# Optimization experiments

Measured on AMD Instinct MI355X. Metric: run time of the kernel, lower is better.

The kernel has to match this reference:

```python
import jax, jax.numpy as jnp
import numpy as np

B, G, IN, H, OUT = 4096, 8, 512, 1024, 64


def setup_inputs() -> dict:
    key = jax.random.key(0)
    k0, k1, k2, k3 = jax.random.split(key, 4)
    x = jax.random.normal(k0, (B, IN), dtype=jnp.float32)
    gid = jax.random.randint(k1, (B,), 0, G, dtype=jnp.int32)
    # Per-group 2-layer MLP params (Kaiming-ish scaling)
    W1 = jax.random.normal(k2, (G, IN, H), dtype=jnp.float32) / np.sqrt(IN)
    b1 = jnp.zeros((G, H), dtype=jnp.float32)
    W2 = jax.random.normal(k3, (G, H, OUT), dtype=jnp.float32) / np.sqrt(H)
    b2 = jnp.zeros((G, OUT), dtype=jnp.float32)
    return {"x": x, "gid": gid, "W1": W1, "b1": b1, "W2": W2, "b2": b2}


def reference(x, gid, W1, b1, W2, b2):
    # Routed 2-layer MLP: each sample i uses expert head gid[i].
    # Compute all G group GEMMs (grouped-GEMM style), then select the
    # routed row per sample with a one-hot contraction (no [B,IN,H]
    # per-sample weight materialization).
    onehot = jax.nn.one_hot(gid, W1.shape[0], dtype=x.dtype)  # [B, G]
    h_all = jnp.einsum('bi,gih->bgh', x, W1) + b1[None]       # [B, G, H]
    h = jax.nn.relu(jnp.einsum('bgh,bg->bh', h_all, onehot))  # [B, H]
    y_all = jnp.einsum('bh,gho->bgo', h, W2) + b2[None]       # [B, G, OUT]
    y = jnp.einsum('bgo,bg->bo', y_all, onehot)               # [B, OUT]
    return y
```

## Files before the change

kernel.cpp:

```cpp
#include <hip/hip_runtime.h>
#include <hip/hip_bf16.h>

#define B_ 4096
#define G_ 8
#define IN_ 512
#define H_ 1024
#define OUT_ 64
#define MAXT 72

typedef float f32x4 __attribute__((ext_vector_type(4)));
typedef __bf16 bf16x8 __attribute__((ext_vector_type(8)));
typedef unsigned short u16x8 __attribute__((ext_vector_type(8)));

__device__ inline unsigned short f2bf(float f) {
  unsigned int u = __builtin_bit_cast(unsigned int, f);
  u += 0x7fffu + ((u >> 16) & 1u);
  return (unsigned short)(u >> 16);
}

__device__ inline u16x8 pack8(float4 a, float4 b) {
  return u16x8{f2bf(a.x), f2bf(a.y), f2bf(a.z), f2bf(a.w),
               f2bf(b.x), f2bf(b.y), f2bf(b.z), f2bf(b.w)};
}

__device__ inline bool tile_lookup(const int* __restrict__ meta, int mt,
                                   int& g, int& row0, int& start, int& cnt) {
  int ts = 0;
  bool found = false;
#pragma unroll
  for (int gg = 0; gg < G_; gg++) {
    int s = meta[gg], e = meta[gg + 1];
    int T = (e - s + 63) >> 6;
    if (!found && mt >= ts && mt < ts + T) {
      g = gg;
      row0 = (mt - ts) << 6;
      start = s;
      cnt = e - s;
      found = true;
    }
    ts += T;
  }
  return found;
}

__global__ __launch_bounds__(256) void prep_kernel(
    const float* __restrict__ W1, const float* __restrict__ W2,
    const float* __restrict__ x, unsigned short* __restrict__ W1t,
    unsigned short* __restrict__ W2t, unsigned short* __restrict__ xb) {
  int b = blockIdx.x;
  int t = threadIdx.x;
  if (b < 4096) {
    __shared__ float tile[32][33];
    int h32 = b & 31, k32 = (b >> 5) & 15, g = b >> 9;
    int kl = t >> 3, nl = (t & 7) * 4;
    const float* src =
        W1 + ((size_t)g * IN_ + k32 * 32 + kl) * H_ + h32 * 32 + nl;
    float4 v = *(const float4*)src;
    tile[kl][nl + 0] = v.x;
    tile[kl][nl + 1] = v.y;
    tile[kl][nl + 2] = v.z;
    tile[kl][nl + 3] = v.w;
    __syncthreads();
    int nl2 = t >> 3, kl2 = (t & 7) * 4;
    ushort4 o;
    o.x = f2bf(tile[kl2 + 0][nl2]);
    o.y = f2bf(tile[kl2 + 1][nl2]);
    o.z = f2bf(tile[kl2 + 2][nl2]);
    o.w = f2bf(tile[kl2 + 3][nl2]);
    *(ushort4*)(W1t + ((size_t)g * H_ + h32 * 32 + nl2) * IN_ + k32 * 32 +
                kl2) = o;
  } else if (b < 4608) {
    __shared__ float tile2[32][33];
    int bb = b - 4096;
    int g = bb >> 6, k32 = (bb >> 1) & 31, n32 = bb & 1;
    int kl = t >> 3, nl = (t & 7) * 4;
    const float* src =
        W2 + ((size_t)g * H_ + k32 * 32 + kl) * OUT_ + n32 * 32 + nl;
    float4 v = *(const float4*)src;
    tile2[kl][nl + 0] = v.x;
    tile2[kl][nl + 1] = v.y;
    tile2[kl][nl + 2] = v.z;
    tile2[kl][nl + 3] = v.w;
    __syncthreads();
    int nl2 = t >> 3, kl2 = (t & 7) * 4;
    ushort4 o;
    o.x = f2bf(tile2[kl2 + 0][nl2]);
    o.y = f2bf(tile2[kl2 + 1][nl2]);
    o.z = f2bf(tile2[kl2 + 2][nl2]);
    o.w = f2bf(tile2[kl2 + 3][nl2]);
    *(ushort4*)(W2t + ((size_t)g * OUT_ + n32 * 32 + nl2) * H_ + k32 * 32 +
                kl2) = o;
  } else {
    int bb = b - 4608;
    size_t base = (size_t)bb * 2048 + t * 8;
    float4 v0 = *(const float4*)(x + base);
    float4 v1 = *(const float4*)(x + base + 4);
    *(u16x8*)(xb + base) = pack8(v0, v1);
  }
}

__global__ __launch_bounds__(256) void bucket_kernel(
    const int* __restrict__ gid, int* __restrict__ meta,
    int* __restrict__ perm) {
  __shared__ unsigned short lc[256][G_];
  __shared__ int offs_s[G_ + 1];
  int t = threadIdx.x;
#pragma unroll
  for (int g = 0; g < G_; g++) lc[t][g] = 0;
  int myg[16];
  const int base = t * 16;
#pragma unroll
  for (int j = 0; j < 16; j++) {
    myg[j] = gid[base + j];
    lc[t][myg[j]]++;
  }
  __syncthreads();
  if (t < G_) {
    int run = 0;
    for (int tt = 0; tt < 256; tt++) {
      int v = lc[tt][t];
      lc[tt][t] = (unsigned short)run;
      run += v;
    }
    offs_s[t + 1] = run;
  }
  __syncthreads();
  if (t == 0) {
    int o = 0;
    for (int g = 0; g < G_; g++) {
      int c = offs_s[g + 1];
      offs_s[g] = o;
      meta[g] = o;
      o += c;
    }
    offs_s[G_] = o;
    meta[G_] = o;
  }
  __syncthreads();
  int cur[G_];
#pragma unroll
  for (int g = 0; g < G_; g++) cur[g] = offs_s[g] + (int)lc[t][g];
#pragma unroll
  for (int j = 0; j < 16; j++) {
    int g = myg[j];
    perm[cur[g]++] = base + j;
  }
}

__global__ __launch_bounds__(256) void gemm1_kernel(
    const unsigned short* __restrict__ xb, const unsigned short* __restrict__ W1t,
    const float* __restrict__ b1, const int* __restrict__ meta,
    const int* __restrict__ perm, unsigned short* __restrict__ hb) {
  int b = blockIdx.x;
  int mt = b >> 4, nt = b & 15;
  int g, row0, start, cnt;
  if (!tile_lookup(meta, mt, g, row0, start, cnt)) return;
  int n0 = nt * 64;

  __shared__ __attribute__((aligned(16))) unsigned short As[64 * 64];
  __shared__ __attribute__((aligned(16))) unsigned short Bs[64 * 64];
  __shared__ int rows[64];

  int tid = threadIdx.x;
  int lane = tid & 63;
  int wv = tid >> 6;

  if (tid < 64) rows[tid] = perm[start + min(row0 + tid, cnt - 1)];
  __syncthreads();

  int r = tid >> 2, c4 = tid & 3;
  const unsigned short* xsrc = xb + (size_t)rows[r] * IN_ + c4 * 16;
  unsigned short* adst0 = &As[r * 64 + (((2 * c4) ^ (r & 7)) << 3)];
  unsigned short* adst1 = &As[r * 64 + (((2 * c4 + 1) ^ (r & 7)) << 3)];

  int brow0 = wv * 16 + (lane >> 3);
  int brow1 = brow0 + 8;
  int bsl = lane & 7;
  const unsigned short* bsrc0 = W1t + ((size_t)g * H_ + n0 + brow0) * IN_ +
                                ((bsl ^ (brow0 & 7)) << 3);
  const unsigned short* bsrc1 = W1t + ((size_t)g * H_ + n0 + brow1) * IN_ +
                                ((bsl ^ (brow1 & 7)) << 3);
  unsigned short* bdst0 = &Bs[wv * 1024 + lane * 8];
  unsigned short* bdst1 = &Bs[wv * 1024 + 512 + lane * 8];

  int fl = lane & 15, q = lane >> 4;
  int m0 = (wv >> 1) * 32, nw = (wv & 1) * 32;
  const unsigned short* apA = &As[(m0 + fl) * 64];
  const unsigned short* apB = &As[(m0 + 16 + fl) * 64];
  const unsigned short* bpA = &Bs[(nw + fl) * 64];
  const unsigned short* bpB = &Bs[(nw + 16 + fl) * 64];

  f32x4 acc[2][2];
#pragma unroll
  for (int i = 0; i < 2; i++)
#pragma unroll
    for (int j = 0; j < 2; j++) acc[i][j] = f32x4{0.f, 0.f, 0.f, 0.f};

  u16x8 av0 = *(const u16x8*)(xsrc + 0);
  u16x8 av1 = *(const u16x8*)(xsrc + 8);

  for (int it = 0; it < 8; it++) {
    int k0 = it * 64;
    u16x8 bw0 = *(const u16x8*)(bsrc0 + k0);
    u16x8 bw1 = *(const u16x8*)(bsrc1 + k0);
    __syncthreads();
    *(u16x8*)adst0 = av0;
    *(u16x8*)adst1 = av1;
    *(u16x8*)bdst0 = bw0;
    *(u16x8*)bdst1 = bw1;
    __syncthreads();
    if (it < 7) {
      int kn = k0 + 64;
      av0 = *(const u16x8*)(xsrc + kn);
      av1 = *(const u16x8*)(xsrc + kn + 8);
    }
#pragma unroll
    for (int s = 0; s < 2; s++) {
      int off = (((s << 2) + q) ^ (fl & 7)) << 3;
      bf16x8 a0 = *(const bf16x8*)(apA + off);
      bf16x8 a1 = *(const bf16x8*)(apB + off);
      bf16x8 fb0 = *(const bf16x8*)(bpA + off);
      bf16x8 fb1 = *(const bf16x8*)(bpB + off);
      acc[0][0] = __builtin_amdgcn_mfma_f32_16x16x32_bf16(a0, fb0, acc[0][0], 0, 0, 0);
      acc[1][0] = __builtin_amdgcn_mfma_f32_16x16x32_bf16(a1, fb0, acc[1][0], 0, 0, 0);
      acc[0][1] = __builtin_amdgcn_mfma_f32_16x16x32_bf16(a0, fb1, acc[0][1], 0, 0, 0);
      acc[1][1] = __builtin_amdgcn_mfma_f32_16x16x32_bf16(a1, fb1, acc[1][1], 0, 0, 0);
    }
  }

#pragma unroll
  for (int ni = 0; ni < 2; ni++) {
    int col = n0 + nw + ni * 16 + fl;
    float bias = b1[g * H_ + col];
#pragma unroll
    for (int mi = 0; mi < 2; mi++) {
#pragma unroll
      for (int rg = 0; rg < 4; rg++) {
        int rl = m0 + mi * 16 + q * 4 + rg;
        if (row0 + rl < cnt) {
          float v = fmaxf(acc[mi][ni][rg] + bias, 0.f);
          hb[(size_t)(start + row0 + rl) * H_ + col] = f2bf(v);
        }
      }
    }
  }
}

__global__ __launch_bounds__(256) void gemm2_kernel(
    const unsigned short* __restrict__ hb, const unsigned short* __restrict__ W2t,
    const float* __restrict__ b2, const int* __restrict__ meta,
    const int* __restrict__ perm, float* __restrict__ y) {
  int mt = blockIdx.x;
  int g, row0, start, cnt;
  if (!tile_lookup(meta, mt, g, row0, start, cnt)) return;

  __shared__ __attribute__((aligned(16))) unsigned short As2[64 * 128];
  __shared__ __attribute__((aligned(16))) unsigned short Bs2[64 * 128];
  __shared__ int rows[64];

  int tid = threadIdx.x;
  int lane = tid & 63;
  int wv = tid >> 6;

  if (tid < 64) rows[tid] = perm[start + min(row0 + tid, cnt - 1)];

  int arow_in_op = lane >> 4;
  int asl = lane & 15;
  const unsigned short* asrc[4];
#pragma unroll
  for (int j = 0; j < 4; j++) {
    int row = wv * 16 + j * 4 + arow_in_op;
    int cs = asl ^ (row & 7);
    asrc[j] = hb + (size_t)(start + min(row0 + row, cnt - 1)) * H_ +
              (cs << 3);
  }

  int bn = tid >> 2, qd = tid & 3;
  const unsigned short* bsrc = W2t + ((size_t)g * OUT_ + bn) * H_ + qd * 32;
  unsigned short* bdst[4];
#pragma unroll
  for (int j = 0; j < 4; j++) {
    int ch = 4 * qd + j;
    bdst[j] = &Bs2[bn * 128 + (((ch ^ (bn & 7)) & 15) << 3)];
  }

  int fl = lane & 15, q = lane >> 4;
  int m0 = (wv >> 1) * 32, nw = (wv & 1) * 32;
  const unsigned short* apA = &As2[(m0 + fl) * 128];
  const unsigned short* apB = &As2[(m0 + 16 + fl) * 128];
  const unsigned short* bpA = &Bs2[(nw + fl) * 128];
  const unsigned short* bpB = &Bs2[(nw + 16 + fl) * 128];

  f32x4 acc[2][2];
#pragma unroll
  for (int i = 0; i < 2; i++)
#pragma unroll
    for (int j = 0; j < 2; j++) acc[i][j] = f32x4{0.f, 0.f, 0.f, 0.f};

  for (int it = 0; it < 8; it++) {
    int kbase = it * 128;
    u16x8 av[4];
#pragma unroll
    for (int j = 0; j < 4; j++) av[j] = *(const u16x8*)(asrc[j] + kbase);
    u16x8 bv[4];
#pragma unroll
    for (int j = 0; j < 4; j++) bv[j] = *(const u16x8*)(bsrc + kbase + j * 8);
    __syncthreads();
#pragma unroll
    for (int j = 0; j < 4; j++)
      *(u16x8*)&As2[(wv * 16 + j * 4) * 128 + lane * 8] = av[j];
#pragma unroll
    for (int j = 0; j < 4; j++) *(u16x8*)bdst[j] = bv[j];
    __syncthreads();
#pragma unroll
    for (int s = 0; s < 4; s++) {
      int off = (((s << 2) + q) ^ (fl & 7)) << 3;
      bf16x8 a0 = *(const bf16x8*)(apA + off);
      bf16x8 a1 = *(const bf16x8*)(apB + off);
      bf16x8 fb0 = *(const bf16x8*)(bpA + off);
      bf16x8 fb1 = *(const bf16x8*)(bpB + off);
      acc[0][0] = __builtin_amdgcn_mfma_f32_16x16x32_bf16(a0, fb0, acc[0][0], 0, 0, 0);
      acc[1][0] = __builtin_amdgcn_mfma_f32_16x16x32_bf16(a1, fb0, acc[1][0], 0, 0, 0);
      acc[0][1] = __builtin_amdgcn_mfma_f32_16x16x32_bf16(a0, fb1, acc[0][1], 0, 0, 0);
      acc[1][1] = __builtin_amdgcn_mfma_f32_16x16x32_bf16(a1, fb1, acc[1][1], 0, 0, 0);
    }
  }

#pragma unroll
  for (int ni = 0; ni < 2; ni++) {
    int col = nw + ni * 16 + fl;
    float bias = b2[g * OUT_ + col];
#pragma unroll
    for (int mi = 0; mi < 2; mi++) {
#pragma unroll
      for (int rg = 0; rg < 4; rg++) {
        int rl = m0 + mi * 16 + q * 4 + rg;
        if (row0 + rl < cnt) {
          y[(size_t)rows[rl] * OUT_ + col] = acc[mi][ni][rg] + bias;
        }
      }
    }
  }
}

extern "C" void kernel_launch(void* const* d_in, const int* in_sizes, int n_in,
                              void* d_out, int out_size, void* d_ws,
                              size_t ws_size, hipStream_t stream) {
  const float* x = (const float*)d_in[0];
  const int* gid = (const int*)d_in[1];
  const float* W1 = (const float*)d_in[2];
  const float* b1 = (const float*)d_in[3];
  const float* W2 = (const float*)d_in[4];
  const float* b2 = (const float*)d_in[5];
  float* y = (float*)d_out;

  int* meta = (int*)d_ws;
  int* perm = (int*)((char*)d_ws + 64);
  unsigned short* W1t = (unsigned short*)((char*)d_ws + (1u << 16));
  unsigned short* W2t = (unsigned short*)((char*)d_ws + (16u << 20));
  unsigned short* xb = (unsigned short*)((char*)d_ws + (24u << 20));
  unsigned short* hb = (unsigned short*)((char*)d_ws + (32u << 20));

  prep_kernel<<<5632, 256, 0, stream>>>(W1, W2, x, W1t, W2t, xb);
  bucket_kernel<<<1, 256, 0, stream>>>(gid, meta, perm);
  gemm1_kernel<<<MAXT * 16, 256, 0, stream>>>(xb, W1t, b1, meta, perm, hb);
  gemm2_kernel<<<MAXT, 256, 0, stream>>>(hb, W2t, b2, meta, perm, y);
}
```

Measured before the change: 114.4 us.

## Double-buffer LDS in both GEMMs and fold bucketing into prep kernel

Both GEMM kernels now use two LDS buffers with a register prefetch two steps ahead, cutting the two barriers per K-step to one so global loads overlap the MFMA work. The single-block bucket kernel becomes an extra block of the prep kernel, which removes one launch. Its serial per-group scan over 256 threads is replaced by a warp-shuffle parallel prefix scan. In exchange, LDS use per block doubles, which may lower occupancy, and register pressure rises from the extra prefetch registers.

After: 109.0 us. 1.05x faster.

```diff
diff --git a/kernel.cpp b/kernel.cpp
--- a/kernel.cpp
+++ b/kernel.cpp
@@ -45,8 +45,10 @@
 
 __global__ __launch_bounds__(256) void prep_kernel(
     const float* __restrict__ W1, const float* __restrict__ W2,
-    const float* __restrict__ x, unsigned short* __restrict__ W1t,
-    unsigned short* __restrict__ W2t, unsigned short* __restrict__ xb) {
+    const float* __restrict__ x, const int* __restrict__ gid,
+    unsigned short* __restrict__ W1t, unsigned short* __restrict__ W2t,
+    unsigned short* __restrict__ xb, int* __restrict__ meta,
+    int* __restrict__ perm) {
   int b = blockIdx.x;
   int t = threadIdx.x;
   if (b < 4096) {
@@ -90,75 +92,83 @@
     o.w = f2bf(tile2[kl2 + 3][nl2]);
     *(ushort4*)(W2t + ((size_t)g * OUT_ + n32 * 32 + nl2) * H_ + k32 * 32 +
                 kl2) = o;
-  } else {
+  } else if (b < 5632) {
     int bb = b - 4608;
     size_t base = (size_t)bb * 2048 + t * 8;
     float4 v0 = *(const float4*)(x + base);
     float4 v1 = *(const float4*)(x + base + 4);
     *(u16x8*)(xb + base) = pack8(v0, v1);
-  }
-}
-
-__global__ __launch_bounds__(256) void bucket_kernel(
-    const int* __restrict__ gid, int* __restrict__ meta,
-    int* __restrict__ perm) {
-  __shared__ unsigned short lc[256][G_];
-  __shared__ int offs_s[G_ + 1];
-  int t = threadIdx.x;
-#pragma unroll
-  for (int g = 0; g < G_; g++) lc[t][g] = 0;
-  int myg[16];
-  const int base = t * 16;
-#pragma unroll
-  for (int j = 0; j < 16; j++) {
-    myg[j] = gid[base + j];
-    lc[t][myg[j]]++;
-  }
-  __syncthreads();
-  if (t < G_) {
-    int run = 0;
-    for (int tt = 0; tt < 256; tt++) {
-      int v = lc[tt][t];
-      lc[tt][t] = (unsigned short)run;
-      run += v;
-    }
-    offs_s[t + 1] = run;
-  }
-  __syncthreads();
-  if (t == 0) {
-    int o = 0;
-    for (int g = 0; g < G_; g++) {
-      int c = offs_s[g + 1];
-      offs_s[g] = o;
-      meta[g] = o;
-      o += c;
-    }
-    offs_s[G_] = o;
-    meta[G_] = o;
-  }
-  __syncthreads();
-  int cur[G_];
-#pragma unroll
-  for (int g = 0; g < G_; g++) cur[g] = offs_s[g] + (int)lc[t][g];
-#pragma unroll
-  for (int j = 0; j < 16; j++) {
-    int g = myg[j];
-    perm[cur[g]++] = base + j;
+  } else {
+    __shared__ unsigned short lc[G_][256];
+    __shared__ int offs_s[G_ + 1];
+#pragma unroll
+    for (int g = 0; g < G_; g++) lc[g][t] = 0;
+    int myg[16];
+    const int base = t * 16;
+#pragma unroll
+    for (int j = 0; j < 16; j++) {
+      myg[j] = gid[base + j];
+      lc[myg[j]][t]++;
+    }
+    __syncthreads();
+    {
+      int g = t >> 5, k = t & 31;
+      unsigned short pref[8];
+      int s = 0;
+#pragma unroll
+      for (int j = 0; j < 8; j++) {
+        pref[j] = (unsigned short)s;
+        s += lc[g][8 * k + j];
+      }
+      int incl = s;
+#pragma unroll
+      for (int d = 1; d < 32; d <<= 1) {
+        int o = __shfl_up(incl, d, 32);
+        if (k >= d) incl += o;
+      }
+      int excl = incl - s;
+      if (k == 31) offs_s[g + 1] = incl;
+#pragma unroll
+      for (int j = 0; j < 8; j++)
+        lc[g][8 * k + j] = (unsigned short)(excl + pref[j]);
+    }
+    __syncthreads();
+    if (t == 0) {
+      int o = 0;
+      for (int g = 0; g < G_; g++) {
+        int c = offs_s[g + 1];
+        offs_s[g] = o;
+        meta[g] = o;
+        o += c;
+      }
+      offs_s[G_] = o;
+      meta[G_] = o;
+    }
+    __syncthreads();
+    int cur[G_];
+#pragma unroll
+    for (int g = 0; g < G_; g++) cur[g] = offs_s[g] + (int)lc[g][t];
+#pragma unroll
+    for (int j = 0; j < 16; j++) {
+      int g = myg[j];
+      perm[cur[g]++] = base + j;
+    }
   }
 }
 
 __global__ __launch_bounds__(256) void gemm1_kernel(
-    const unsigned short* __restrict__ xb, const unsigned short* __restrict__ W1t,
-    const float* __restrict__ b1, const int* __restrict__ meta,
-    const int* __restrict__ perm, unsigned short* __restrict__ hb) {
+    const unsigned short* __restrict__ xb,
+    const unsigned short* __restrict__ W1t, const float* __restrict__ b1,
+    const int* __restrict__ meta, const int* __restrict__ perm,
+    unsigned short* __restrict__ hb) {
   int b = blockIdx.x;
   int mt = b >> 4, nt = b & 15;
   int g, row0, start, cnt;
   if (!tile_lookup(meta, mt, g, row0, start, cnt)) return;
   int n0 = nt * 64;
 
-  __shared__ __attribute__((aligned(16))) unsigned short As[64 * 64];
-  __shared__ __attribute__((aligned(16))) unsigned short Bs[64 * 64];
+  __shared__ __attribute__((aligned(16))) unsigned short As[2][64 * 64];
+  __shared__ __attribute__((aligned(16))) unsigned short Bs[2][64 * 64];
   __shared__ int rows[64];
 
   int tid = threadIdx.x;
@@ -170,8 +180,8 @@
 
   int r = tid >> 2, c4 = tid & 3;
   const unsigned short* xsrc = xb + (size_t)rows[r] * IN_ + c4 * 16;
-  unsigned short* adst0 = &As[r * 64 + (((2 * c4) ^ (r & 7)) << 3)];
-  unsigned short* adst1 = &As[r * 64 + (((2 * c4 + 1) ^ (r & 7)) << 3)];
+  int aoff0 = r * 64 + (((2 * c4) ^ (r & 7)) << 3);
+  int aoff1 = r * 64 + (((2 * c4 + 1) ^ (r & 7)) << 3);
 
   int brow0 = wv * 16 + (lane >> 3);
   int brow1 = brow0 + 8;
@@ -180,15 +190,15 @@
                                 ((bsl ^ (brow0 & 7)) << 3);
   const unsigned short* bsrc1 = W1t + ((size_t)g * H_ + n0 + brow1) * IN_ +
                                 ((bsl ^ (brow1 & 7)) << 3);
-  unsigned short* bdst0 = &Bs[wv * 1024 + lane * 8];
-  unsigned short* bdst1 = &Bs[wv * 1024 + 512 + lane * 8];
+  int boff0 = wv * 1024 + lane * 8;
+  int boff1 = wv * 1024 + 512 + lane * 8;
 
   int fl = lane & 15, q = lane >> 4;
   int m0 = (wv >> 1) * 32, nw = (wv & 1) * 32;
-  const unsigned short* apA = &As[(m0 + fl) * 64];
-  const unsigned short* apB = &As[(m0 + 16 + fl) * 64];
-  const unsigned short* bpA = &Bs[(nw + fl) * 64];
-  const unsigned short* bpB = &Bs[(nw + 16 + fl) * 64];
+  int apA = (m0 + fl) * 64;
+  int apB = (m0 + 16 + fl) * 64;
+  int bpA = (nw + fl) * 64;
+  int bpB = (nw + 16 + fl) * 64;
 
   f32x4 acc[2][2];
 #pragma unroll
@@ -198,34 +208,46 @@
 
   u16x8 av0 = *(const u16x8*)(xsrc + 0);
   u16x8 av1 = *(const u16x8*)(xsrc + 8);
+  u16x8 bw0 = *(const u16x8*)(bsrc0 + 0);
+  u16x8 bw1 = *(const u16x8*)(bsrc1 + 0);
+  *(u16x8*)&As[0][aoff0] = av0;
+  *(u16x8*)&As[0][aoff1] = av1;
+  *(u16x8*)&Bs[0][boff0] = bw0;
+  *(u16x8*)&Bs[0][boff1] = bw1;
+  av0 = *(const u16x8*)(xsrc + 64);
+  av1 = *(const u16x8*)(xsrc + 64 + 8);
+  bw0 = *(const u16x8*)(bsrc0 + 64);
+  bw1 = *(const u16x8*)(bsrc1 + 64);
+  __syncthreads();
 
   for (int it = 0; it < 8; it++) {
-    int k0 = it * 64;
-    u16x8 bw0 = *(const u16x8*)(bsrc0 + k0);
-    u16x8 bw1 = *(const u16x8*)(bsrc1 + k0);
-    __syncthreads();
-    *(u16x8*)adst0 = av0;
-    *(u16x8*)adst1 = av1;
-    *(u16x8*)bdst0 = bw0;
-    *(u16x8*)bdst1 = bw1;
-    __syncthreads();
+    int p = it & 1;
     if (it < 7) {
-      int kn = k0 + 64;
+      *(u16x8*)&As[p ^ 1][aoff0] = av0;
+      *(u16x8*)&As[p ^ 1][aoff1] = av1;
+      *(u16x8*)&Bs[p ^ 1][boff0] = bw0;
+      *(u16x8*)&Bs[p ^ 1][boff1] = bw1;
+    }
+    if (it < 6) {
+      int kn = (it + 2) * 64;
       av0 = *(const u16x8*)(xsrc + kn);
       av1 = *(const u16x8*)(xsrc + kn + 8);
+      bw0 = *(const u16x8*)(bsrc0 + kn);
+      bw1 = *(const u16x8*)(bsrc1 + kn);
     }
 #pragma unroll
     for (int s = 0; s < 2; s++) {
       int off = (((s << 2) + q) ^ (fl & 7)) << 3;
-      bf16x8 a0 = *(const bf16x8*)(apA + off);
-      bf16x8 a1 = *(const bf16x8*)(apB + off);
-      bf16x8 fb0 = *(const bf16x8*)(bpA + off);
-      bf16x8 fb1 = *(const bf16x8*)(bpB + off);
+      bf16x8 a0 = *(const bf16x8*)&As[p][apA + off];
+      bf16x8 a1 = *(const bf16x8*)&As[p][apB + off];
+      bf16x8 fb0 = *(const bf16x8*)&Bs[p][bpA + off];
+      bf16x8 fb1 = *(const bf16x8*)&Bs[p][bpB + off];
       acc[0][0] = __builtin_amdgcn_mfma_f32_16x16x32_bf16(a0, fb0, acc[0][0], 0, 0, 0);
       acc[1][0] = __builtin_amdgcn_mfma_f32_16x16x32_bf16(a1, fb0, acc[1][0], 0, 0, 0);
       acc[0][1] = __builtin_amdgcn_mfma_f32_16x16x32_bf16(a0, fb1, acc[0][1], 0, 0, 0);
       acc[1][1] = __builtin_amdgcn_mfma_f32_16x16x32_bf16(a1, fb1, acc[1][1], 0, 0, 0);
     }
+    __syncthreads();
   }
 
 #pragma unroll
@@ -247,15 +269,16 @@
 }
 
 __global__ __launch_bounds__(256) void gemm2_kernel(
-    const unsigned short* __restrict__ hb, const unsigned short* __restrict__ W2t,
-    const float* __restrict__ b2, const int* __restrict__ meta,
-    const int* __restrict__ perm, float* __restrict__ y) {
+    const unsigned short* __restrict__ hb,
+    const unsigned short* __restrict__ W2t, const float* __restrict__ b2,
+    const int* __restrict__ meta, const int* __restrict__ perm,
+    float* __restrict__ y) {
   int mt = blockIdx.x;
   int g, row0, start, cnt;
   if (!tile_lookup(meta, mt, g, row0, start, cnt)) return;
 
-  __shared__ __attribute__((aligned(16))) unsigned short As2[64 * 128];
-  __shared__ __attribute__((aligned(16))) unsigned short Bs2[64 * 128];
+  __shared__ __attribute__((aligned(16))) unsigned short As2[2][64 * 128];
+  __shared__ __attribute__((aligned(16))) unsigned short Bs2[2][64 * 128];
   __shared__ int rows[64];
 
   int tid = threadIdx.x;
@@ -267,29 +290,31 @@
   int arow_in_op = lane >> 4;
   int asl = lane & 15;
   const unsigned short* asrc[4];
+  int adst[4];
 #pragma unroll
   for (int j = 0; j < 4; j++) {
     int row = wv * 16 + j * 4 + arow_in_op;
     int cs = asl ^ (row & 7);
-    asrc[j] = hb + (size_t)(start + min(row0 + row, cnt - 1)) * H_ +
-              (cs << 3);
+    asrc[j] =
+        hb + (size_t)(start + min(row0 + row, cnt - 1)) * H_ + (cs << 3);
+    adst[j] = (wv * 16 + j * 4) * 128 + lane * 8;
   }
 
   int bn = tid >> 2, qd = tid & 3;
   const unsigned short* bsrc = W2t + ((size_t)g * OUT_ + bn) * H_ + qd * 32;
-  unsigned short* bdst[4];
+  int bdst[4];
 #pragma unroll
   for (int j = 0; j < 4; j++) {
     int ch = 4 * qd + j;
-    bdst[j] = &Bs2[bn * 128 + (((ch ^ (bn & 7)) & 15) << 3)];
+    bdst[j] = bn * 128 + ((ch ^ (bn & 7)) << 3);
   }
 
   int fl = lane & 15, q = lane >> 4;
   int m0 = (wv >> 1) * 32, nw = (wv & 1) * 32;
-  const unsigned short* apA = &As2[(m0 + fl) * 128];
-  const unsigned short* apB = &As2[(m0 + 16 + fl) * 128];
-  const unsigned short* bpA = &Bs2[(nw + fl) * 128];
-  const unsigned short* bpB = &Bs2[(nw + 16 + fl) * 128];
+  int apA = (m0 + fl) * 128;
+  int apB = (m0 + 16 + fl) * 128;
+  int bpA = (nw + fl) * 128;
+  int bpB = (nw + 16 + fl) * 128;
 
   f32x4 acc[2][2];
 #pragma unroll
@@ -297,33 +322,50 @@
 #pragma unroll
     for (int j = 0; j < 2; j++) acc[i][j] = f32x4{0.f, 0.f, 0.f, 0.f};
 
+  u16x8 av[4], bv[4];
+#pragma unroll
+  for (int j = 0; j < 4; j++) av[j] = *(const u16x8*)(asrc[j] + 0);
+#pragma unroll
+  for (int j = 0; j < 4; j++) bv[j] = *(const u16x8*)(bsrc + j * 8);
+#pragma unroll
+  for (int j = 0; j < 4; j++) *(u16x8*)&As2[0][adst[j]] = av[j];
+#pragma unroll
+  for (int j = 0; j < 4; j++) *(u16x8*)&Bs2[0][bdst[j]] = bv[j];
+#pragma unroll
+  for (int j = 0; j < 4; j++) av[j] = *(const u16x8*)(asrc[j] + 128);
+#pragma unroll
+  for (int j = 0; j < 4; j++) bv[j] = *(const u16x8*)(bsrc + 128 + j * 8);
+  __syncthreads();
+
   for (int it = 0; it < 8; it++) {
-    int kbase = it * 128;
-    u16x8 av[4];
-#pragma unroll
-    for (int j = 0; j < 4; j++) av[j] = *(const u16x8*)(asrc[j] + kbase);
-    u16x8 bv[4];
-#pragma unroll
-    for (int j = 0; j < 4; j++) bv[j] = *(const u16x8*)(bsrc + kbase + j * 8);
-    __syncthreads();
-#pragma unroll
-    for (int j = 0; j < 4; j++)
-      *(u16x8*)&As2[(wv * 16 + j * 4) * 128 + lane * 8] = av[j];
-#pragma unroll
-    for (int j = 0; j < 4; j++) *(u16x8*)bdst[j] = bv[j];
-    __syncthreads();
+    int p = it & 1;
+    if (it < 7) {
+#pragma unroll
+      for (int j = 0; j < 4; j++) *(u16x8*)&As2[p ^ 1][adst[j]] = av[j];
+#pragma unroll
+      for (int j = 0; j < 4; j++) *(u16x8*)&Bs2[p ^ 1][bdst[j]] = bv[j];
+    }
+    if (it < 6) {
+      int kn = (it + 2) * 128;
+#pragma unroll
+      for (int j = 0; j < 4; j++) av[j] = *(const u16x8*)(asrc[j] + kn);
+#pragma unroll
+      for (int j = 0; j < 4; j++)
+        bv[j] = *(const u16x8*)(bsrc + kn + j * 8);
+    }
 #pragma unroll
     for (int s = 0; s < 4; s++) {
       int off = (((s << 2) + q) ^ (fl & 7)) << 3;
-      bf16x8 a0 = *(const bf16x8*)(apA + off);
-      bf16x8 a1 = *(const bf16x8*)(apB + off);
-      bf16x8 fb0 = *(const bf16x8*)(bpA + off);
-      bf16x8 fb1 = *(const bf16x8*)(bpB + off);
+      bf16x8 a0 = *(const bf16x8*)&As2[p][apA + off];
+      bf16x8 a1 = *(const bf16x8*)&As2[p][apB + off];
+      bf16x8 fb0 = *(const bf16x8*)&Bs2[p][bpA + off];
+      bf16x8 fb1 = *(const bf16x8*)&Bs2[p][bpB + off];
       acc[0][0] = __builtin_amdgcn_mfma_f32_16x16x32_bf16(a0, fb0, acc[0][0], 0, 0, 0);
       acc[1][0] = __builtin_amdgcn_mfma_f32_16x16x32_bf16(a1, fb0, acc[1][0], 0, 0, 0);
       acc[0][1] = __builtin_amdgcn_mfma_f32_16x16x32_bf16(a0, fb1, acc[0][1], 0, 0, 0);
       acc[1][1] = __builtin_amdgcn_mfma_f32_16x16x32_bf16(a1, fb1, acc[1][1], 0, 0, 0);
     }
+    __syncthreads();
   }
 
 #pragma unroll
@@ -361,8 +403,8 @@
   unsigned short* xb = (unsigned short*)((char*)d_ws + (24u << 20));
   unsigned short* hb = (unsigned short*)((char*)d_ws + (32u << 20));
 
-  prep_kernel<<<5632, 256, 0, stream>>>(W1, W2, x, W1t, W2t, xb);
-  bucket_kernel<<<1, 256, 0, stream>>>(gid, meta, perm);
+  prep_kernel<<<5633, 256, 0, stream>>>(W1, W2, x, gid, W1t, W2t, xb, meta,
+                                        perm);
   gemm1_kernel<<<MAXT * 16, 256, 0, stream>>>(xb, W1t, b1, meta, perm, hb);
   gemm2_kernel<<<MAXT, 256, 0, stream>>>(hb, W2t, b2, meta, perm, y);
 }
```
